# Kernel optimization log

Hardware: AMD Instinct MI355X
Metric: run time of the kernel (lower is better)

The kernel has to match this reference:

```python
import jax, jax.numpy as jnp
import numpy as np
import math

B, S, D, H = 4, 1024, 1024, 16
DK = D // H


def setup_inputs() -> dict:
    key = jax.random.key(0)
    ks = jax.random.split(key, 14)
    inp = {
        "query": jax.random.normal(ks[0], (B, S, D), dtype=jnp.float32),
        "key": jax.random.normal(ks[1], (B, S, D), dtype=jnp.float32),
        "value": jax.random.normal(ks[2], (B, S, D), dtype=jnp.float32),
        "attention_bias": jax.random.normal(ks[3], (B, S, S, H), dtype=jnp.float32),
        "mask": jax.random.randint(ks[4], (B, S), 0, 2).astype(bool),
    }
    scale = 0.02
    inp["Wq"] = jax.random.normal(ks[5], (D, D), dtype=jnp.float32) * scale
    inp["bq"] = jnp.zeros((D,), dtype=jnp.float32)
    inp["Wk"] = jax.random.normal(ks[6], (D, D), dtype=jnp.float32) * scale
    inp["bk"] = jnp.zeros((D,), dtype=jnp.float32)
    inp["Wv"] = jax.random.normal(ks[7], (D, D), dtype=jnp.float32) * scale
    inp["bv"] = jnp.zeros((D,), dtype=jnp.float32)
    inp["Wo"] = jax.random.normal(ks[8], (D, D), dtype=jnp.float32) * scale
    inp["bo"] = jnp.zeros((D,), dtype=jnp.float32)
    return inp


def reference(query, key, value, attention_bias, mask, Wq, bq, Wk, bk, Wv, bv, Wo, bo):
    # projections (torch Linear: x @ W.T + b), split heads -> [B,H,S,DK]
    def proj(x, W, b):
        y = x @ W.T + b
        return y.reshape(B, S, H, DK).transpose(0, 2, 1, 3)

    q = proj(query, Wq, bq)
    k = proj(key, Wk, bk)
    v = proj(value, Wv, bv)

    bias = attention_bias.transpose(0, 3, 1, 2)  # [B,H,S,S]
    scores = (jnp.einsum("bhqd,bhkd->bhqk", q, k) + bias) / math.sqrt(DK)

    # pairwise mask: outer product of per-token mask, broadcast over heads
    pm = (mask[:, None, :, None] & mask[:, None, None, :])  # [B,1,S,S]
    scores = jnp.where(pm, scores, jnp.float32(-1e9))

    p_attn = jax.nn.softmax(scores, axis=-1)  # dropout is identity in eval
    x = jnp.einsum("bhqk,bhkd->bhqd", p_attn, v)
    x = x.transpose(0, 2, 1, 3).reshape(B, S, D)
    return x @ Wo.T + bo
```

## Files before the change

kernel.cpp:

```cpp
#include <hip/hip_runtime.h>
#include <hip/hip_bf16.h>
#include <math.h>

#define B_ 4
#define S_ 1024
#define D_ 1024
#define H_ 16
#define DK_ 64

typedef short bf16x8 __attribute__((ext_vector_type(8)));
typedef float f32x4 __attribute__((ext_vector_type(4)));

#define MFMA(a, b, c) __builtin_amdgcn_mfma_f32_16x16x32_bf16(a, b, c, 0, 0, 0)

#define GLDS(gp, lp)                                                        \
    __builtin_amdgcn_global_load_lds(                                       \
        (const __attribute__((address_space(1))) void*)(const void*)(gp),   \
        (__attribute__((address_space(3))) void*)(void*)(lp), 16, 0, 0)

static __device__ __forceinline__ unsigned short f2bf(float f) {
    __hip_bfloat16 h = __float2bfloat16(f);
    return *reinterpret_cast<unsigned short*>(&h);
}
static __device__ __forceinline__ float bf2f(unsigned short u) {
    unsigned int x = ((unsigned int)u) << 16;
    union { unsigned int i; float f; } c; c.i = x; return c.f;
}

__global__ __launch_bounds__(256) void cvt3(
    const float* __restrict__ a, const float* __restrict__ b, const float* __restrict__ c,
    unsigned short* __restrict__ oa, unsigned short* __restrict__ ob, unsigned short* __restrict__ oc)
{
    int bx = blockIdx.x;
    int which = bx >> 12;
    const float* in = which == 0 ? a : which == 1 ? b : c;
    unsigned short* out = which == 0 ? oa : which == 1 ? ob : oc;
    int i = (bx & 4095) * 256 + threadIdx.x;
    float4 v = ((const float4*)in)[i];
    ushort4 o;
    o.x = f2bf(v.x); o.y = f2bf(v.y); o.z = f2bf(v.z); o.w = f2bf(v.w);
    ((ushort4*)out)[i] = o;
}

__global__ __launch_bounds__(256) void cvt4(
    const float* __restrict__ a, const float* __restrict__ b,
    const float* __restrict__ c, const float* __restrict__ d,
    unsigned short* __restrict__ oa, unsigned short* __restrict__ ob,
    unsigned short* __restrict__ oc, unsigned short* __restrict__ od)
{
    int bx = blockIdx.x;
    int which = bx >> 10;
    const float* in = which == 0 ? a : which == 1 ? b : which == 2 ? c : d;
    unsigned short* out = which == 0 ? oa : which == 1 ? ob : which == 2 ? oc : od;
    int i = (bx & 1023) * 256 + threadIdx.x;
    float4 v = ((const float4*)in)[i];
    ushort4 o;
    o.x = f2bf(v.x); o.y = f2bf(v.y); o.z = f2bf(v.z); o.w = f2bf(v.w);
    ((ushort4*)out)[i] = o;
}

__global__ __launch_bounds__(256) void prep_bias(
    const float* __restrict__ bias, const int* __restrict__ mask,
    unsigned short* __restrict__ biasP)
{
    const int t = threadIdx.x;
    const int h = t & 15, u = t >> 4;
    const int x = blockIdx.x;
    const int kt = x & 15, q16 = (x >> 4) & 63, b = x >> 10;

    const unsigned short NEG = f2bf(-28672.f);

    int mk[4];
    #pragma unroll
    for (int j = 0; j < 4; ++j) mk[j] = mask[b * 1024 + kt * 64 + j * 16 + u];

    const float* bb = bias + (((size_t)(b * 1024 + q16 * 16) * 1024) + kt * 64) * 16 + h;
    unsigned short* ob = biasP + ((((size_t)(b * 16 + h) * 64 + q16) * 16 + kt) * 64) * 16;

    #pragma unroll
    for (int quad = 0; quad < 4; ++quad) {
        bf16x8 v0, v1;
        #pragma unroll
        for (int r = 0; r < 4; ++r) {
            int q = quad * 4 + r;
            int mq = mask[b * 1024 + q16 * 16 + q];
            #pragma unroll
            for (int j = 0; j < 4; ++j) {
                float v = bb[((size_t)q * 1024 + j * 16 + u) * 16];
                unsigned short pv = (mq && mk[j]) ? f2bf(v * 0.125f) : NEG;
                if (j < 2) v0[j * 4 + r] = (short)pv;
                else       v1[(j - 2) * 4 + r] = (short)pv;
            }
        }
        unsigned short* dst = ob + (size_t)(quad * 16 + u) * 16;
        *(bf16x8*)(dst) = v0;
        *(bf16x8*)(dst + 8) = v1;
    }
}

__global__ __launch_bounds__(256, 2) void gemm128(
    const unsigned short* __restrict__ X0, const unsigned short* __restrict__ X1,
    const unsigned short* __restrict__ X2,
    const unsigned short* __restrict__ W0, const unsigned short* __restrict__ W1,
    const unsigned short* __restrict__ W2,
    const float* __restrict__ bv0, const float* __restrict__ bv1,
    const float* __restrict__ bv2,
    void* __restrict__ Y0, void* __restrict__ Y1, void* __restrict__ Y2,
    const int* __restrict__ mask, int mode_ovr)
{
    __shared__ unsigned short As[128 * 32];
    __shared__ unsigned short Bs[128 * 32];

    const int z = blockIdx.z;
    const unsigned short* X = z == 0 ? X0 : z == 1 ? X1 : X2;
    const unsigned short* W = z == 0 ? W0 : z == 1 ? W1 : W2;
    const float* bvec = z == 0 ? bv0 : z == 1 ? bv1 : bv2;
    void* Yv = z == 0 ? Y0 : z == 1 ? Y1 : Y2;
    const int mode = mode_ovr >= 0 ? mode_ovr : z;

    const int t = threadIdx.x;
    const int w = t >> 6, l = t & 63;
    const int lane16 = l & 15, quad = l >> 4;
    const int m0 = blockIdx.y * 128, n0 = blockIdx.x * 128;
    const int wr = w >> 1, wc = w & 1;

    const int srow = w * 16 + (l >> 2);
    const unsigned short* agp = X + (size_t)(m0 + srow) * 1024 + (l & 3) * 8;
    const unsigned short* bgp = W + (size_t)(n0 + srow) * 1024 + (l & 3) * 8;
    unsigned short* alp = As + w * 512 + l * 8;
    unsigned short* blp = Bs + w * 512 + l * 8;

    f32x4 zero = {0.f, 0.f, 0.f, 0.f};
    f32x4 acc[4][4];
    #pragma unroll
    for (int i = 0; i < 4; ++i)
        #pragma unroll
        for (int j = 0; j < 4; ++j) acc[i][j] = zero;

    for (int kt = 0; kt < 1024; kt += 32) {
        GLDS(agp + kt, alp);
        GLDS(agp + kt + 64 * 1024, alp + 2048);
        GLDS(bgp + kt, blp);
        GLDS(bgp + kt + 64 * 1024, blp + 2048);
        __syncthreads();

        bf16x8 af[4], bfv[4];
        #pragma unroll
        for (int i = 0; i < 4; ++i)
            af[i] = *(const bf16x8*)(As + (wr * 64 + i * 16 + lane16) * 32 + quad * 8);
        #pragma unroll
        for (int j = 0; j < 4; ++j)
            bfv[j] = *(const bf16x8*)(Bs + (wc * 64 + j * 16 + lane16) * 32 + quad * 8);

        #pragma unroll
        for (int i = 0; i < 4; ++i)
            #pragma unroll
            for (int j = 0; j < 4; ++j)
                acc[i][j] = MFMA(af[i], bfv[j], acc[i][j]);
        __syncthreads();
    }

    float bvl[4];
    #pragma unroll
    for (int j = 0; j < 4; ++j) bvl[j] = bvec[n0 + wc * 64 + j * 16 + lane16];

    if (mode == 2) {
        const int bb = m0 >> 10;
        const int sb = (m0 & 1023) + wr * 64;
        #pragma unroll
        for (int i = 0; i < 4; ++i) {
            #pragma unroll
            for (int j = 0; j < 4; ++j) {
                int n = n0 + wc * 64 + j * 16 + lane16;
                ushort4 pk;
                pk.x = f2bf(acc[i][j][0] + bvl[j]);
                pk.y = f2bf(acc[i][j][1] + bvl[j]);
                pk.z = f2bf(acc[i][j][2] + bvl[j]);
                pk.w = f2bf(acc[i][j][3] + bvl[j]);
                int s = sb + i * 16 + quad * 4;
                *(ushort4*)((unsigned short*)Yv + ((size_t)(bb * 1024 + n)) * 1024 + s) = pk;
            }
        }
    } else if (mode == 3) {
        float* Y = (float*)Yv;
        #pragma unroll
        for (int i = 0; i < 4; ++i)
            #pragma unroll
            for (int j = 0; j < 4; ++j) {
                int n = n0 + wc * 64 + j * 16 + lane16;
                #pragma unroll
                for (int r = 0; r < 4; ++r) {
                    size_t m = m0 + wr * 64 + i * 16 + quad * 4 + r;
                    Y[m * 1024 + n] = acc[i][j][r] + bvl[j];
                }
            }
    } else {
        unsigned short* Y = (unsigned short*)Yv;
        #pragma unroll
        for (int i = 0; i < 4; ++i) {
            int mrow[4];
            #pragma unroll
            for (int r = 0; r < 4; ++r)
                mrow[r] = (mode == 0) ? mask[m0 + wr * 64 + i * 16 + quad * 4 + r] : 1;
            #pragma unroll
            for (int j = 0; j < 4; ++j) {
                int n = n0 + wc * 64 + j * 16 + lane16;
                #pragma unroll
                for (int r = 0; r < 4; ++r) {
                    size_t m = m0 + wr * 64 + i * 16 + quad * 4 + r;
                    float val = acc[i][j][r] + bvl[j];
                    if (mode == 0) val = mrow[r] ? val * 0.125f : 0.f;
                    Y[m * 1024 + n] = f2bf(val);
                }
            }
        }
    }
}

__global__ __launch_bounds__(256, 2) void attn_mfma(
    const unsigned short* __restrict__ Qp, const unsigned short* __restrict__ Kp,
    const unsigned short* __restrict__ VpT, const unsigned short* __restrict__ biasP,
    unsigned short* __restrict__ Xp)
{
    __shared__ unsigned short Ks[64 * 64];
    __shared__ unsigned short Vs[64 * 64];
    __shared__ unsigned short Ps[4][16 * 72];

    const int t = threadIdx.x;
    const int w = t >> 6, l = t & 63;
    const int lane16 = l & 15, quad = l >> 4;

    const int bid = blockIdx.x;
    const int bh = bid & 63, qt = bid >> 6;
    const int h = bh & 15, b = bh >> 4;
    const int q0 = qt * 64;
    const int qrow0 = q0 + w * 16;
    const int q16 = qt * 4 + w;

    bf16x8 qf[2];
    #pragma unroll
    for (int c = 0; c < 2; ++c)
        qf[c] = *(const bf16x8*)(Qp + (size_t)(b * 1024 + qrow0 + lane16) * 1024
                                 + h * 64 + c * 32 + quad * 8);

    const unsigned short* bp = biasP
        + ((((size_t)(b * 16 + h) * 64 + q16) * 16) * 64 + l) * 16;

    const int krow = w * 8 + (l >> 3);
    const int kgran = (l & 7) ^ ((l >> 3) & 7);
    const unsigned short* kg = Kp + (size_t)(b * 1024 + krow) * 1024 + h * 64 + kgran * 8;
    unsigned short* klp = Ks + w * 512 + l * 8;
    const unsigned short* vg = VpT + ((size_t)(b * 16 + h) * 64 + krow) * 1024 + kgran * 8;
    unsigned short* vlp = Vs + w * 512 + l * 8;

    f32x4 zero = {0.f, 0.f, 0.f, 0.f};
    f32x4 o[4];
    #pragma unroll
    for (int j = 0; j < 4; ++j) o[j] = zero;
    float m_i[4] = {-1e30f, -1e30f, -1e30f, -1e30f};
    float l_i[4] = {0.f, 0.f, 0.f, 0.f};

    for (int kt16 = 0; kt16 < 16; ++kt16) {
        const int k0 = kt16 * 64;
        GLDS(kg + (size_t)k0 * 1024, klp);
        GLDS(kg + (size_t)(k0 + 32) * 1024, klp + 32 * 64);
        GLDS(vg + k0, vlp);
        GLDS(vg + k0 + 32 * 1024, vlp + 32 * 64);

        bf16x8 bfr0 = *(const bf16x8*)(bp + (size_t)kt16 * 1024);
        bf16x8 bfr1 = *(const bf16x8*)(bp + (size_t)kt16 * 1024 + 8);
        __syncthreads();

        f32x4 s[4];
        #pragma unroll
        for (int j = 0; j < 4; ++j) {
            s[j] = zero;
            #pragma unroll
            for (int c = 0; c < 2; ++c) {
                bf16x8 kf = *(const bf16x8*)(Ks + (j * 16 + lane16) * 64
                                             + (((c * 4 + quad) ^ (lane16 & 7)) * 8));
                s[j] = MFMA(qf[c], kf, s[j]);
            }
        }

        float sc[4][4];
        #pragma unroll
        for (int e = 0; e < 8; ++e) {
            sc[e >> 2][e & 3]       = s[e >> 2][e & 3]       + bf2f((unsigned short)bfr0[e]);
            sc[2 + (e >> 2)][e & 3] = s[2 + (e >> 2)][e & 3] + bf2f((unsigned short)bfr1[e]);
        }

        float p[4][4];
        #pragma unroll
        for (int r = 0; r < 4; ++r) {
            float mx = fmaxf(fmaxf(sc[0][r], sc[1][r]), fmaxf(sc[2][r], sc[3][r]));
            #pragma unroll
            for (int d = 1; d < 16; d <<= 1) mx = fmaxf(mx, __shfl_xor(mx, d, 64));
            float mnew = fmaxf(m_i[r], mx);
            float alpha = __expf(m_i[r] - mnew);
            m_i[r] = mnew;
            float sum = 0.f;
            #pragma unroll
            for (int j = 0; j < 4; ++j) {
                p[j][r] = __expf(sc[j][r] - mnew);
                sum += p[j][r];
            }
            #pragma unroll
            for (int d = 1; d < 16; d <<= 1) sum += __shfl_xor(sum, d, 64);
            l_i[r] = l_i[r] * alpha + sum;
            #pragma unroll
            for (int jd = 0; jd < 4; ++jd) o[jd][r] *= alpha;
        }

        #pragma unroll
        for (int j = 0; j < 4; ++j)
            #pragma unroll
            for (int r = 0; r < 4; ++r)
                Ps[w][(quad * 4 + r) * 72 + j * 16 + lane16] = f2bf(p[j][r]);
        asm volatile("" ::: "memory");

        bf16x8 pf[2];
        #pragma unroll
        for (int c = 0; c < 2; ++c)
            pf[c] = *(const bf16x8*)(&Ps[w][lane16 * 72 + c * 32 + quad * 8]);

        #pragma unroll
        for (int jd = 0; jd < 4; ++jd)
            #pragma unroll
            for (int c = 0; c < 2; ++c) {
                bf16x8 vf = *(const bf16x8*)(Vs + (jd * 16 + lane16) * 64
                                             + (((c * 4 + quad) ^ (lane16 & 7)) * 8));
                o[jd] = MFMA(pf[c], vf, o[jd]);
            }
        __syncthreads();
    }

    float inv[4];
    #pragma unroll
    for (int r = 0; r < 4; ++r) inv[r] = 1.0f / l_i[r];

    #pragma unroll
    for (int jd = 0; jd < 4; ++jd)
        #pragma unroll
        for (int r = 0; r < 4; ++r)
            Xp[(size_t)(b * 1024 + qrow0 + quad * 4 + r) * 1024
               + h * 64 + jd * 16 + lane16] = f2bf(o[jd][r] * inv[r]);
}

extern "C" void kernel_launch(void* const* d_in, const int* in_sizes, int n_in,
                              void* d_out, int out_size, void* d_ws, size_t ws_size,
                              hipStream_t stream)
{
    const float* query = (const float*)d_in[0];
    const float* key   = (const float*)d_in[1];
    const float* value = (const float*)d_in[2];
    const float* abias = (const float*)d_in[3];
    const int*   mask  = (const int*)d_in[4];
    const float* Wq = (const float*)d_in[5];
    const float* bq = (const float*)d_in[6];
    const float* Wk = (const float*)d_in[7];
    const float* bk = (const float*)d_in[8];
    const float* Wv = (const float*)d_in[9];
    const float* bv = (const float*)d_in[10];
    const float* Wo = (const float*)d_in[11];
    const float* bo = (const float*)d_in[12];
    float* out = (float*)d_out;

    const size_t T = (size_t)B_ * S_ * D_;
    const size_t WSZ = (size_t)D_ * D_;
    const size_t BPSZ = (size_t)B_ * H_ * S_ * S_;
    unsigned short* p = (unsigned short*)d_ws;
    unsigned short* biasP = p;  p += BPSZ;
    unsigned short* qb  = p;  p += T;
    unsigned short* kb  = p;  p += T;
    unsigned short* vb  = p;  p += T;
    unsigned short* wqb = p;  p += WSZ;
    unsigned short* wkb = p;  p += WSZ;
    unsigned short* wvb = p;  p += WSZ;
    unsigned short* wob = p;  p += WSZ;
    unsigned short* Qpj = p;  p += T;
    unsigned short* Kpj = p;  p += T;
    unsigned short* VpT = p;  p += T;
    unsigned short* Xpj = p;  p += T;

    cvt3<<<dim3(3 * 4096), 256, 0, stream>>>(query, key, value, qb, kb, vb);
    cvt4<<<dim3(4 * 1024), 256, 0, stream>>>(Wq, Wk, Wv, Wo, wqb, wkb, wvb, wob);
    prep_bias<<<dim3(4096), 256, 0, stream>>>(abias, mask, biasP);

    gemm128<<<dim3(8, 32, 3), 256, 0, stream>>>(
        qb, kb, vb, wqb, wkb, wvb, bq, bk, bv,
        (void*)Qpj, (void*)Kpj, (void*)VpT, mask, -1);

    attn_mfma<<<dim3(1024), 256, 0, stream>>>(Qpj, Kpj, VpT, biasP, Xpj);

    gemm128<<<dim3(8, 32, 1), 256, 0, stream>>>(
        Xpj, Xpj, Xpj, wob, wob, wob, bo, bo, bo,
        (void*)out, (void*)out, (void*)out, mask, 3);
}
```

Baseline: 582.9 us.

## Fuse bias/mask prep into attention kernel with all-heads-per-block tiling

Removes the separate prep_bias pass and the bf16 biasP workspace; the attention kernel now reads the fp32 [B,S,S,H] bias directly, scaling and masking it inline. Each 512-thread block handles 16 query rows across all 16 heads (two heads per wave), so a bias row's contiguous head values are read once as packed pairs. K and V tiles for all heads are staged in LDS per 32-key step. This trades an extra full bias read-modify-write for larger LDS use (about 128KB per block) and only 256 blocks, which risks low occupancy and poor latency hiding.

New measurement: 668.9 us. 14.7% more time.

```diff
diff --git a/kernel.cpp b/kernel.cpp
--- a/kernel.cpp
+++ b/kernel.cpp
@@ -21,10 +21,6 @@
 static __device__ __forceinline__ unsigned short f2bf(float f) {
     __hip_bfloat16 h = __float2bfloat16(f);
     return *reinterpret_cast<unsigned short*>(&h);
-}
-static __device__ __forceinline__ float bf2f(unsigned short u) {
-    unsigned int x = ((unsigned int)u) << 16;
-    union { unsigned int i; float f; } c; c.i = x; return c.f;
 }
 
 __global__ __launch_bounds__(256) void cvt3(
@@ -59,45 +55,6 @@
     ((ushort4*)out)[i] = o;
 }
 
-__global__ __launch_bounds__(256) void prep_bias(
-    const float* __restrict__ bias, const int* __restrict__ mask,
-    unsigned short* __restrict__ biasP)
-{
-    const int t = threadIdx.x;
-    const int h = t & 15, u = t >> 4;
-    const int x = blockIdx.x;
-    const int kt = x & 15, q16 = (x >> 4) & 63, b = x >> 10;
-
-    const unsigned short NEG = f2bf(-28672.f);
-
-    int mk[4];
-    #pragma unroll
-    for (int j = 0; j < 4; ++j) mk[j] = mask[b * 1024 + kt * 64 + j * 16 + u];
-
-    const float* bb = bias + (((size_t)(b * 1024 + q16 * 16) * 1024) + kt * 64) * 16 + h;
-    unsigned short* ob = biasP + ((((size_t)(b * 16 + h) * 64 + q16) * 16 + kt) * 64) * 16;
-
-    #pragma unroll
-    for (int quad = 0; quad < 4; ++quad) {
-        bf16x8 v0, v1;
-        #pragma unroll
-        for (int r = 0; r < 4; ++r) {
-            int q = quad * 4 + r;
-            int mq = mask[b * 1024 + q16 * 16 + q];
-            #pragma unroll
-            for (int j = 0; j < 4; ++j) {
-                float v = bb[((size_t)q * 1024 + j * 16 + u) * 16];
-                unsigned short pv = (mq && mk[j]) ? f2bf(v * 0.125f) : NEG;
-                if (j < 2) v0[j * 4 + r] = (short)pv;
-                else       v1[(j - 2) * 4 + r] = (short)pv;
-            }
-        }
-        unsigned short* dst = ob + (size_t)(quad * 16 + u) * 16;
-        *(bf16x8*)(dst) = v0;
-        *(bf16x8*)(dst + 8) = v1;
-    }
-}
-
 __global__ __launch_bounds__(256, 2) void gemm128(
     const unsigned short* __restrict__ X0, const unsigned short* __restrict__ X1,
     const unsigned short* __restrict__ X2,
@@ -217,134 +174,158 @@
     }
 }
 
-__global__ __launch_bounds__(256, 2) void attn_mfma(
+__global__ __launch_bounds__(512, 2) void attn_mfma2(
     const unsigned short* __restrict__ Qp, const unsigned short* __restrict__ Kp,
-    const unsigned short* __restrict__ VpT, const unsigned short* __restrict__ biasP,
-    unsigned short* __restrict__ Xp)
-{
-    __shared__ unsigned short Ks[64 * 64];
-    __shared__ unsigned short Vs[64 * 64];
-    __shared__ unsigned short Ps[4][16 * 72];
+    const unsigned short* __restrict__ VpT, const float* __restrict__ bias,
+    const int* __restrict__ mask, unsigned short* __restrict__ Xp)
+{
+    __shared__ unsigned short Ks[32 * 1024];
+    __shared__ unsigned short Vs[1024 * 32];
+    __shared__ unsigned short Ps[8][16 * 72];
 
     const int t = threadIdx.x;
     const int w = t >> 6, l = t & 63;
     const int lane16 = l & 15, quad = l >> 4;
 
     const int bid = blockIdx.x;
-    const int bh = bid & 63, qt = bid >> 6;
-    const int h = bh & 15, b = bh >> 4;
-    const int q0 = qt * 64;
-    const int qrow0 = q0 + w * 16;
-    const int q16 = qt * 4 + w;
-
-    bf16x8 qf[2];
-    #pragma unroll
-    for (int c = 0; c < 2; ++c)
-        qf[c] = *(const bf16x8*)(Qp + (size_t)(b * 1024 + qrow0 + lane16) * 1024
-                                 + h * 64 + c * 32 + quad * 8);
-
-    const unsigned short* bp = biasP
-        + ((((size_t)(b * 16 + h) * 64 + q16) * 16) * 64 + l) * 16;
-
-    const int krow = w * 8 + (l >> 3);
-    const int kgran = (l & 7) ^ ((l >> 3) & 7);
-    const unsigned short* kg = Kp + (size_t)(b * 1024 + krow) * 1024 + h * 64 + kgran * 8;
-    unsigned short* klp = Ks + w * 512 + l * 8;
-    const unsigned short* vg = VpT + ((size_t)(b * 16 + h) * 64 + krow) * 1024 + kgran * 8;
-    unsigned short* vlp = Vs + w * 512 + l * 8;
+    const int b = bid & 3, qt = bid >> 2;
+    const int q0 = qt * 16;
+    const int h0 = w * 2;
+
+    bf16x8 qf[2][2];
+    #pragma unroll
+    for (int hh = 0; hh < 2; ++hh)
+        #pragma unroll
+        for (int c = 0; c < 2; ++c)
+            qf[hh][c] = *(const bf16x8*)(Qp + (size_t)(b * 1024 + q0 + lane16) * 1024
+                                         + (h0 + hh) * 64 + c * 32 + quad * 8);
+
+    int mq[4];
+    #pragma unroll
+    for (int r = 0; r < 4; ++r) mq[r] = mask[b * 1024 + q0 + quad * 4 + r];
+
+    const float* brp[4];
+    #pragma unroll
+    for (int r = 0; r < 4; ++r)
+        brp[r] = bias + ((size_t)(b * 1024 + q0 + quad * 4 + r) * 1024 + lane16) * 16 + h0;
 
     f32x4 zero = {0.f, 0.f, 0.f, 0.f};
-    f32x4 o[4];
-    #pragma unroll
-    for (int j = 0; j < 4; ++j) o[j] = zero;
-    float m_i[4] = {-1e30f, -1e30f, -1e30f, -1e30f};
-    float l_i[4] = {0.f, 0.f, 0.f, 0.f};
-
-    for (int kt16 = 0; kt16 < 16; ++kt16) {
-        const int k0 = kt16 * 64;
-        GLDS(kg + (size_t)k0 * 1024, klp);
-        GLDS(kg + (size_t)(k0 + 32) * 1024, klp + 32 * 64);
-        GLDS(vg + k0, vlp);
-        GLDS(vg + k0 + 32 * 1024, vlp + 32 * 64);
-
-        bf16x8 bfr0 = *(const bf16x8*)(bp + (size_t)kt16 * 1024);
-        bf16x8 bfr1 = *(const bf16x8*)(bp + (size_t)kt16 * 1024 + 8);
+    f32x4 o[2][4];
+    float m_i[2][4], l_i[2][4];
+    #pragma unroll
+    for (int hh = 0; hh < 2; ++hh)
+        #pragma unroll
+        for (int r = 0; r < 4; ++r) {
+            m_i[hh][r] = -1e30f; l_i[hh][r] = 0.f;
+            o[hh][r] = zero;
+        }
+
+    for (int kt = 0; kt < 32; ++kt) {
+        const int k0 = kt * 32;
+
+        #pragma unroll
+        for (int i = 0; i < 8; ++i) {
+            int row = w * 4 + (i >> 1), half = i & 1;
+            GLDS(Kp + (size_t)(b * 1024 + k0 + row) * 1024
+                    + (half * 64 + (l ^ (row & 7))) * 8,
+                 Ks + row * 1024 + half * 512);
+        }
+        #pragma unroll
+        for (int i = 0; i < 8; ++i) {
+            int vr0 = w * 128 + i * 16;
+            GLDS(VpT + (size_t)(b * 1024 + vr0 + (l >> 2)) * 1024 + k0 + (l & 3) * 8,
+                 Vs + vr0 * 32);
+        }
+
+        int mk[2];
+        double bvd[2][4];
+        #pragma unroll
+        for (int j = 0; j < 2; ++j) {
+            mk[j] = mask[b * 1024 + k0 + j * 16 + lane16];
+            #pragma unroll
+            for (int r = 0; r < 4; ++r)
+                bvd[j][r] = __builtin_nontemporal_load(
+                    (const double*)(brp[r] + (size_t)(k0 + j * 16) * 16));
+        }
         __syncthreads();
 
-        f32x4 s[4];
-        #pragma unroll
-        for (int j = 0; j < 4; ++j) {
-            s[j] = zero;
-            #pragma unroll
-            for (int c = 0; c < 2; ++c) {
-                bf16x8 kf = *(const bf16x8*)(Ks + (j * 16 + lane16) * 64
-                                             + (((c * 4 + quad) ^ (lane16 & 7)) * 8));
-                s[j] = MFMA(qf[c], kf, s[j]);
-            }
-        }
-
-        float sc[4][4];
-        #pragma unroll
-        for (int e = 0; e < 8; ++e) {
-            sc[e >> 2][e & 3]       = s[e >> 2][e & 3]       + bf2f((unsigned short)bfr0[e]);
-            sc[2 + (e >> 2)][e & 3] = s[2 + (e >> 2)][e & 3] + bf2f((unsigned short)bfr1[e]);
-        }
-
-        float p[4][4];
-        #pragma unroll
-        for (int r = 0; r < 4; ++r) {
-            float mx = fmaxf(fmaxf(sc[0][r], sc[1][r]), fmaxf(sc[2][r], sc[3][r]));
-            #pragma unroll
-            for (int d = 1; d < 16; d <<= 1) mx = fmaxf(mx, __shfl_xor(mx, d, 64));
-            float mnew = fmaxf(m_i[r], mx);
-            float alpha = __expf(m_i[r] - mnew);
-            m_i[r] = mnew;
-            float sum = 0.f;
-            #pragma unroll
-            for (int j = 0; j < 4; ++j) {
-                p[j][r] = __expf(sc[j][r] - mnew);
-                sum += p[j][r];
-            }
-            #pragma unroll
-            for (int d = 1; d < 16; d <<= 1) sum += __shfl_xor(sum, d, 64);
-            l_i[r] = l_i[r] * alpha + sum;
-            #pragma unroll
-            for (int jd = 0; jd < 4; ++jd) o[jd][r] *= alpha;
-        }
-
-        #pragma unroll
-        for (int j = 0; j < 4; ++j)
-            #pragma unroll
-            for (int r = 0; r < 4; ++r)
-                Ps[w][(quad * 4 + r) * 72 + j * 16 + lane16] = f2bf(p[j][r]);
-        asm volatile("" ::: "memory");
-
-        bf16x8 pf[2];
-        #pragma unroll
-        for (int c = 0; c < 2; ++c)
-            pf[c] = *(const bf16x8*)(&Ps[w][lane16 * 72 + c * 32 + quad * 8]);
-
-        #pragma unroll
-        for (int jd = 0; jd < 4; ++jd)
-            #pragma unroll
-            for (int c = 0; c < 2; ++c) {
-                bf16x8 vf = *(const bf16x8*)(Vs + (jd * 16 + lane16) * 64
-                                             + (((c * 4 + quad) ^ (lane16 & 7)) * 8));
-                o[jd] = MFMA(pf[c], vf, o[jd]);
-            }
+        f32x4 s[2][2];
+        #pragma unroll
+        for (int hh = 0; hh < 2; ++hh)
+            #pragma unroll
+            for (int j = 0; j < 2; ++j) {
+                s[hh][j] = zero;
+                #pragma unroll
+                for (int c = 0; c < 2; ++c) {
+                    bf16x8 kf = *(const bf16x8*)(Ks + (j * 16 + lane16) * 1024
+                        + ((h0 + hh) * 8 + ((c * 4 + quad) ^ (lane16 & 7))) * 8);
+                    s[hh][j] = MFMA(qf[hh][c], kf, s[hh][j]);
+                }
+            }
+
+        #pragma unroll
+        for (int hh = 0; hh < 2; ++hh) {
+            float sc[2][4];
+            #pragma unroll
+            for (int j = 0; j < 2; ++j)
+                #pragma unroll
+                for (int r = 0; r < 4; ++r) {
+                    union { double d; float2 f; } u; u.d = bvd[j][r];
+                    float bv = hh ? u.f.y : u.f.x;
+                    float v = fmaf(bv, 0.125f, s[hh][j][r]);
+                    sc[j][r] = (mq[r] && mk[j]) ? v : -1e9f;
+                }
+
+            float p[2][4];
+            #pragma unroll
+            for (int r = 0; r < 4; ++r) {
+                float mx = fmaxf(sc[0][r], sc[1][r]);
+                #pragma unroll
+                for (int d = 1; d < 16; d <<= 1) mx = fmaxf(mx, __shfl_xor(mx, d, 64));
+                float mnew = fmaxf(m_i[hh][r], mx);
+                float alpha = __expf(m_i[hh][r] - mnew);
+                m_i[hh][r] = mnew;
+                p[0][r] = __expf(sc[0][r] - mnew);
+                p[1][r] = __expf(sc[1][r] - mnew);
+                float sum = p[0][r] + p[1][r];
+                #pragma unroll
+                for (int d = 1; d < 16; d <<= 1) sum += __shfl_xor(sum, d, 64);
+                l_i[hh][r] = l_i[hh][r] * alpha + sum;
+                #pragma unroll
+                for (int jd = 0; jd < 4; ++jd) o[hh][jd][r] *= alpha;
+            }
+
+            #pragma unroll
+            for (int j = 0; j < 2; ++j)
+                #pragma unroll
+                for (int r = 0; r < 4; ++r)
+                    Ps[w][(quad * 4 + r) * 72 + j * 16 + lane16] = f2bf(p[j][r]);
+            asm volatile("" ::: "memory");
+            bf16x8 pf = *(const bf16x8*)(&Ps[w][lane16 * 72 + quad * 8]);
+            asm volatile("" ::: "memory");
+
+            #pragma unroll
+            for (int jd = 0; jd < 4; ++jd) {
+                bf16x8 vf = *(const bf16x8*)(Vs + ((h0 + hh) * 64 + jd * 16 + lane16) * 32
+                                             + quad * 8);
+                o[hh][jd] = MFMA(pf, vf, o[hh][jd]);
+            }
+        }
         __syncthreads();
     }
 
-    float inv[4];
-    #pragma unroll
-    for (int r = 0; r < 4; ++r) inv[r] = 1.0f / l_i[r];
-
-    #pragma unroll
-    for (int jd = 0; jd < 4; ++jd)
-        #pragma unroll
-        for (int r = 0; r < 4; ++r)
-            Xp[(size_t)(b * 1024 + qrow0 + quad * 4 + r) * 1024
-               + h * 64 + jd * 16 + lane16] = f2bf(o[jd][r] * inv[r]);
+    #pragma unroll
+    for (int hh = 0; hh < 2; ++hh) {
+        float inv[4];
+        #pragma unroll
+        for (int r = 0; r < 4; ++r) inv[r] = 1.0f / l_i[hh][r];
+        #pragma unroll
+        for (int jd = 0; jd < 4; ++jd)
+            #pragma unroll
+            for (int r = 0; r < 4; ++r)
+                Xp[(size_t)(b * 1024 + q0 + quad * 4 + r) * 1024
+                   + (h0 + hh) * 64 + jd * 16 + lane16] = f2bf(o[hh][jd][r] * inv[r]);
+    }
 }
 
 extern "C" void kernel_launch(void* const* d_in, const int* in_sizes, int n_in,
@@ -368,9 +349,7 @@
 
     const size_t T = (size_t)B_ * S_ * D_;
     const size_t WSZ = (size_t)D_ * D_;
-    const size_t BPSZ = (size_t)B_ * H_ * S_ * S_;
     unsigned short* p = (unsigned short*)d_ws;
-    unsigned short* biasP = p;  p += BPSZ;
     unsigned short* qb  = p;  p += T;
     unsigned short* kb  = p;  p += T;
     unsigned short* vb  = p;  p += T;
@@ -385,13 +364,12 @@
 
     cvt3<<<dim3(3 * 4096), 256, 0, stream>>>(query, key, value, qb, kb, vb);
     cvt4<<<dim3(4 * 1024), 256, 0, stream>>>(Wq, Wk, Wv, Wo, wqb, wkb, wvb, wob);
-    prep_bias<<<dim3(4096), 256, 0, stream>>>(abias, mask, biasP);
 
     gemm128<<<dim3(8, 32, 3), 256, 0, stream>>>(
         qb, kb, vb, wqb, wkb, wvb, bq, bk, bv,
         (void*)Qpj, (void*)Kpj, (void*)VpT, mask, -1);
 
-    attn_mfma<<<dim3(1024), 256, 0, stream>>>(Qpj, Kpj, VpT, biasP, Xpj);
+    attn_mfma2<<<dim3(256), 512, 0, stream>>>(Qpj, Kpj, VpT, abias, mask, Xpj);
 
     gemm128<<<dim3(8, 32, 1), 256, 0, stream>>>(
         Xpj, Xpj, Xpj, wob, wob, wob, bo, bo, bo,
```
